# Kernel optimization log

Measured on AMD Instinct MI355X. Metric: run time of the kernel, lower is better.

Reference implementation:

```python
import jax, jax.numpy as jnp
import numpy as np

ROPE_THETA = 10000.0

def rope(x):
    # x: [B, H, T, D], D even. Standard rotate-half rotary embedding.
    T, D = x.shape[-2], x.shape[-1]
    half = D // 2
    inv_freq = 1.0 / (ROPE_THETA ** (jnp.arange(half, dtype=x.dtype) / half))
    ang = jnp.arange(T, dtype=x.dtype)[:, None] * inv_freq[None, :]  # [T, half]
    cos, sin = jnp.cos(ang), jnp.sin(ang)
    x1, x2 = x[..., :half], x[..., half:]
    return jnp.concatenate([x1 * cos - x2 * sin, x1 * sin + x2 * cos], axis=-1)


def setup_inputs() -> dict:
    key = jax.random.key(0)
    kq, kk, kv = jax.random.split(key, 3)
    shape = (2, 8, 4096, 64)  # [B, H, T, D]
    return {
        "Q": jax.random.normal(kq, shape, dtype=jnp.float32),
        "K": jax.random.normal(kk, shape, dtype=jnp.float32),
        "V": jax.random.normal(kv, shape, dtype=jnp.float32),
    }


def reference(Q, K, V):
    # Unnormalized causal linear attention with RoPE:
    #   tril(RoPE(Q) @ RoPE(K)^T, diagonal=-1) @ V
    Qr = rope(Q)
    Kr = rope(K)
    scores = jnp.einsum("bhqd,bhkd->bhqk", Qr, Kr)  # [B,H,T,T]
    T = scores.shape[-1]
    # strictly lower triangular (diagonal=-1): keep q_idx > k_idx
    mask = jnp.arange(T)[:, None] > jnp.arange(T)[None, :]
    scores = jnp.where(mask, scores, jnp.zeros((), dtype=scores.dtype))
    return jnp.einsum("bhqk,bhkd->bhqd", scores, V)
```

## Files before the change

### kernel.cpp

```cpp
#include <hip/hip_runtime.h>

#define G 16
#define T 4096
#define DD 64
#define NB 64

typedef __attribute__((ext_vector_type(8))) short bf16x8;
typedef __attribute__((ext_vector_type(4))) float f32x4;
typedef unsigned short U16;

__device__ __forceinline__ float bf2f(U16 u) {
  union { unsigned int u; float f; } x; x.u = ((unsigned int)u) << 16; return x.f;
}
__device__ __forceinline__ U16 f2bf(float f) {
  union { float f; unsigned int u; } x; x.f = f;
  unsigned int r = x.u + 0x7FFFu + ((x.u >> 16) & 1u);
  return (U16)(r >> 16);
}

#define MFMA(a, b, c) __builtin_amdgcn_mfma_f32_16x16x32_bf16((a), (b), (c), 0, 0, 0)

#define ROPE_C 0.28782313662425575f

__global__ __launch_bounds__(256) void k_tab(float2* __restrict__ tab) {
  int idx = blockIdx.x * 256 + threadIdx.x;
  int t = idx >> 5, j = idx & 31;
  float invf = expf(-(float)j * ROPE_C);
  float ang = (float)t * invf;
  tab[idx] = make_float2(cosf(ang), sinf(ang));
}

__global__ __launch_bounds__(256) void k_phase1(const float* __restrict__ K, const float* __restrict__ V,
                                                const float2* __restrict__ tab,
                                                U16* __restrict__ Kr, U16* __restrict__ Xu) {
  __shared__ __align__(16) U16 KrT[64][72];
  __shared__ __align__(16) U16 VT[64][72];
  int wid = blockIdx.x;
  int g = wid >> 6, b = wid & 63;
  int k0 = b * 64;
  int tid = threadIdx.x;

  {
    int r = tid >> 2, qq = tid & 3, d0 = qq * 8;
    int t = k0 + r;
    size_t base = ((size_t)g * T + t) * DD;
    const float* rp = K + base;
    const float2* tp = tab + t * 32 + d0;
    float x1[8], x2[8];
    *(float4*)&x1[0] = *(const float4*)(rp + d0);
    *(float4*)&x1[4] = *(const float4*)(rp + d0 + 4);
    *(float4*)&x2[0] = *(const float4*)(rp + d0 + 32);
    *(float4*)&x2[4] = *(const float4*)(rp + d0 + 36);
    bf16x8 v1, v2;
#pragma unroll
    for (int i = 0; i < 8; ++i) {
      float2 cs = tp[i];
      float o1 = x1[i] * cs.x - x2[i] * cs.y;
      float o2 = x1[i] * cs.y + x2[i] * cs.x;
      U16 b1 = f2bf(o1), b2 = f2bf(o2);
      v1[i] = (short)b1; v2[i] = (short)b2;
      KrT[d0 + i][r]      = b1;
      KrT[d0 + i + 32][r] = b2;
    }
    *(bf16x8*)(Kr + base + d0)      = v1;
    *(bf16x8*)(Kr + base + d0 + 32) = v2;
  }
  {
    int c = tid & 63, r0 = (tid >> 6) * 16;
#pragma unroll
    for (int h = 0; h < 2; ++h) {
      bf16x8 tv;
#pragma unroll
      for (int i = 0; i < 8; ++i)
        tv[i] = (short)f2bf(V[((size_t)g * T + k0 + r0 + h * 8 + i) * DD + c]);
      *(bf16x8*)&VT[c][r0 + h * 8] = tv;
    }
  }
  __syncthreads();

  int lane = tid & 63, wv = tid >> 6;
  int lr = lane & 15, lg = lane >> 4;
  bf16x8 A0 = *(const bf16x8*)&VT[16 * wv + lr][8 * lg];
  bf16x8 A1 = *(const bf16x8*)&VT[16 * wv + lr][8 * lg + 32];
#pragma unroll
  for (int dt = 0; dt < 4; ++dt) {
    bf16x8 B0 = *(const bf16x8*)&KrT[16 * dt + lr][8 * lg];
    bf16x8 B1 = *(const bf16x8*)&KrT[16 * dt + lr][8 * lg + 32];
    f32x4 acc = {0.f, 0.f, 0.f, 0.f};
    acc = MFMA(A0, B0, acc);
    acc = MFMA(A1, B1, acc);
#pragma unroll
    for (int rr = 0; rr < 4; ++rr) {
      int e = 16 * wv + 4 * lg + rr, d = 16 * dt + lr;
      Xu[((size_t)wid << 12) + e * 64 + d] = f2bf(acc[rr]);
    }
  }
}

__global__ __launch_bounds__(256) void k_phase2(U16* __restrict__ Xu) {
  int g = blockIdx.x >> 4, slice = blockIdx.x & 15;
  int e = slice * 256 + threadIdx.x;
  size_t base = ((size_t)g << 18) + e;
  float run = 0.f;
#pragma unroll
  for (int grp = 0; grp < 8; ++grp) {
    U16 v[8];
#pragma unroll
    for (int i = 0; i < 8; ++i)
      v[i] = Xu[base + ((size_t)(grp * 8 + i) << 12)];
#pragma unroll
    for (int i = 0; i < 8; ++i) {
      float f = bf2f(v[i]);
      Xu[base + ((size_t)(grp * 8 + i) << 12)] = f2bf(run);
      run += f;
    }
  }
}

__global__ __launch_bounds__(256) void k_phase3(const float* __restrict__ Q, const U16* __restrict__ Kr,
                                                const float* __restrict__ V, const U16* __restrict__ Xu,
                                                const float2* __restrict__ tab,
                                                float* __restrict__ Out) {
  __shared__ __align__(16) U16 SP[64][72];
  __shared__ __align__(16) U16 VT[64][72];
  __shared__ __align__(16) U16 SW[4][16][72];
  int wid = blockIdx.x;
  int g = wid >> 6, b = wid & 63;
  int k0 = b * 64;
  int tid = threadIdx.x;

  {
    int r = tid >> 2, c0 = (tid & 3) * 16;
    const U16* src = Xu + ((size_t)wid << 12) + r * 64 + c0;
    *(bf16x8*)&SP[r][c0]     = *(const bf16x8*)src;
    *(bf16x8*)&SP[r][c0 + 8] = *(const bf16x8*)(src + 8);
  }
  {
    int c = tid & 63, r0 = (tid >> 6) * 16;
#pragma unroll
    for (int h = 0; h < 2; ++h) {
      bf16x8 tv;
#pragma unroll
      for (int i = 0; i < 8; ++i)
        tv[i] = (short)f2bf(V[((size_t)g * T + k0 + r0 + h * 8 + i) * DD + c]);
      *(bf16x8*)&VT[c][r0 + h * 8] = tv;
    }
  }

  int lane = tid & 63, wv = tid >> 6;
  int lr = lane & 15, lg = lane >> 4;
  int q0 = k0 + 16 * wv;

  bf16x8 Aq0, Aq1;
  {
    int t = q0 + lr;
    const float* qrow = Q + ((size_t)g * T + t) * DD;
    const float2* tp = tab + t * 32 + 8 * lg;
    float x1[8], x2[8];
    *(float4*)&x1[0] = *(const float4*)(qrow + 8 * lg);
    *(float4*)&x1[4] = *(const float4*)(qrow + 8 * lg + 4);
    *(float4*)&x2[0] = *(const float4*)(qrow + 8 * lg + 32);
    *(float4*)&x2[4] = *(const float4*)(qrow + 8 * lg + 36);
#pragma unroll
    for (int i = 0; i < 8; ++i) {
      float2 cs = tp[i];
      Aq0[i] = (short)f2bf(x1[i] * cs.x - x2[i] * cs.y);
      Aq1[i] = (short)f2bf(x1[i] * cs.y + x2[i] * cs.x);
    }
  }
  __syncthreads();

  f32x4 O[4];
#pragma unroll
  for (int et = 0; et < 4; ++et) O[et] = (f32x4){0.f, 0.f, 0.f, 0.f};

#pragma unroll
  for (int et = 0; et < 4; ++et) {
    bf16x8 B0 = *(const bf16x8*)&SP[16 * et + lr][8 * lg];
    bf16x8 B1 = *(const bf16x8*)&SP[16 * et + lr][8 * lg + 32];
    O[et] = MFMA(Aq0, B0, O[et]);
    O[et] = MFMA(Aq1, B1, O[et]);
  }

  for (int kt = 0; kt <= wv; ++kt) {
    const U16* krow = Kr + ((size_t)g * T + k0 + 16 * kt + lr) * DD;
    bf16x8 Bk0 = *(const bf16x8*)(krow + 8 * lg);
    bf16x8 Bk1 = *(const bf16x8*)(krow + 8 * lg + 32);
    f32x4 s = {0.f, 0.f, 0.f, 0.f};
    s = MFMA(Aq0, Bk0, s);
    s = MFMA(Aq1, Bk1, s);
#pragma unroll
    for (int rr = 0; rr < 4; ++rr) {
      int qi = 16 * wv + 4 * lg + rr, ki = 16 * kt + lr;
      float val = (qi > ki) ? s[rr] : 0.f;
      SW[wv][4 * lg + rr][16 * kt + lr] = f2bf(val);
    }
  }
  for (int kt = wv + 1; kt < 4; ++kt) {
#pragma unroll
    for (int rr = 0; rr < 4; ++rr)
      SW[wv][4 * lg + rr][16 * kt + lr] = 0;
  }

  bf16x8 As0 = *(const bf16x8*)&SW[wv][lr][8 * lg];
  bf16x8 As1 = *(const bf16x8*)&SW[wv][lr][8 * lg + 32];

#pragma unroll
  for (int et = 0; et < 4; ++et) {
    bf16x8 Bv0 = *(const bf16x8*)&VT[16 * et + lr][8 * lg];
    bf16x8 Bv1 = *(const bf16x8*)&VT[16 * et + lr][8 * lg + 32];
    O[et] = MFMA(As0, Bv0, O[et]);
    O[et] = MFMA(As1, Bv1, O[et]);
  }

#pragma unroll
  for (int et = 0; et < 4; ++et)
#pragma unroll
    for (int rr = 0; rr < 4; ++rr)
      Out[((size_t)g * T + q0 + 4 * lg + rr) * DD + 16 * et + lr] = O[et][rr];
}

extern "C" void kernel_launch(void* const* d_in, const int* in_sizes, int n_in,
                              void* d_out, int out_size, void* d_ws, size_t ws_size,
                              hipStream_t stream) {
  const float* Q = (const float*)d_in[0];
  const float* K = (const float*)d_in[1];
  const float* V = (const float*)d_in[2];
  float* Out = (float*)d_out;
  U16* W  = (U16*)d_ws;
  U16* Kr = W;
  U16* Xu = W + 4194304;
  float2* tab = (float2*)(W + 8388608);
  k_tab<<<512, 256, 0, stream>>>(tab);
  k_phase1<<<G * NB, 256, 0, stream>>>(K, V, tab, Kr, Xu);
  k_phase2<<<256, 256, 0, stream>>>(Xu);
  k_phase3<<<G * NB, 256, 0, stream>>>(Q, Kr, V, Xu, tab, Out);
}
```

Measured before the change: 35.74 us.

## Compute RoPE inline, cache bf16 V, parallelize prefix scan across segments

Drops the separate cos/sin table kernel and computes the RoPE angles inline with fast __expf/__sincosf intrinsics, saving a launch and the table reads. Phase 1 now loads V with coalesced row vectors and writes a bf16 copy, which phase 3 reads instead of reconverting the fp32 V with strided loads. The prefix-sum kernel splits each 64-step chain into 4 segments of 16 combined by shuffles, giving four times more threads and a shorter serial chain. The fast trig intrinsics lose accuracy at large angles (t up to 4095), and the extra workspace buffer adds write traffic.

```diff
diff --git a/kernel.cpp b/kernel.cpp
--- a/kernel.cpp
+++ b/kernel.cpp
@@ -3,7 +3,6 @@
 #define G 16
 #define T 4096
 #define DD 64
-#define NB 64
 
 typedef __attribute__((ext_vector_type(8))) short bf16x8;
 typedef __attribute__((ext_vector_type(4))) float f32x4;
@@ -22,17 +21,9 @@
 
 #define ROPE_C 0.28782313662425575f
 
-__global__ __launch_bounds__(256) void k_tab(float2* __restrict__ tab) {
-  int idx = blockIdx.x * 256 + threadIdx.x;
-  int t = idx >> 5, j = idx & 31;
-  float invf = expf(-(float)j * ROPE_C);
-  float ang = (float)t * invf;
-  tab[idx] = make_float2(cosf(ang), sinf(ang));
-}
-
 __global__ __launch_bounds__(256) void k_phase1(const float* __restrict__ K, const float* __restrict__ V,
-                                                const float2* __restrict__ tab,
-                                                U16* __restrict__ Kr, U16* __restrict__ Xu) {
+                                                U16* __restrict__ Kr, U16* __restrict__ Vb,
+                                                U16* __restrict__ Xu) {
   __shared__ __align__(16) U16 KrT[64][72];
   __shared__ __align__(16) U16 VT[64][72];
   int wid = blockIdx.x;
@@ -40,12 +31,12 @@
   int k0 = b * 64;
   int tid = threadIdx.x;
 
-  {
-    int r = tid >> 2, qq = tid & 3, d0 = qq * 8;
-    int t = k0 + r;
-    size_t base = ((size_t)g * T + t) * DD;
+  int r = tid >> 2, qq = tid & 3, d0 = qq * 8;
+  int t = k0 + r;
+  size_t base = ((size_t)g * T + t) * DD;
+
+  {
     const float* rp = K + base;
-    const float2* tp = tab + t * 32 + d0;
     float x1[8], x2[8];
     *(float4*)&x1[0] = *(const float4*)(rp + d0);
     *(float4*)&x1[4] = *(const float4*)(rp + d0 + 4);
@@ -54,9 +45,12 @@
     bf16x8 v1, v2;
 #pragma unroll
     for (int i = 0; i < 8; ++i) {
-      float2 cs = tp[i];
-      float o1 = x1[i] * cs.x - x2[i] * cs.y;
-      float o2 = x1[i] * cs.y + x2[i] * cs.x;
+      float invf = __expf(-(float)(d0 + i) * ROPE_C);
+      float ang = (float)t * invf;
+      float s, c;
+      __sincosf(ang, &s, &c);
+      float o1 = x1[i] * c - x2[i] * s;
+      float o2 = x1[i] * s + x2[i] * c;
       U16 b1 = f2bf(o1), b2 = f2bf(o2);
       v1[i] = (short)b1; v2[i] = (short)b2;
       KrT[d0 + i][r]      = b1;
@@ -66,15 +60,22 @@
     *(bf16x8*)(Kr + base + d0 + 32) = v2;
   }
   {
-    int c = tid & 63, r0 = (tid >> 6) * 16;
-#pragma unroll
-    for (int h = 0; h < 2; ++h) {
-      bf16x8 tv;
-#pragma unroll
-      for (int i = 0; i < 8; ++i)
-        tv[i] = (short)f2bf(V[((size_t)g * T + k0 + r0 + h * 8 + i) * DD + c]);
-      *(bf16x8*)&VT[c][r0 + h * 8] = tv;
-    }
+    const float* vp = V + base;
+    float y1[8], y2[8];
+    *(float4*)&y1[0] = *(const float4*)(vp + d0);
+    *(float4*)&y1[4] = *(const float4*)(vp + d0 + 4);
+    *(float4*)&y2[0] = *(const float4*)(vp + d0 + 32);
+    *(float4*)&y2[4] = *(const float4*)(vp + d0 + 36);
+    bf16x8 w1, w2;
+#pragma unroll
+    for (int i = 0; i < 8; ++i) {
+      U16 b1 = f2bf(y1[i]), b2 = f2bf(y2[i]);
+      w1[i] = (short)b1; w2[i] = (short)b2;
+      VT[d0 + i][r]      = b1;
+      VT[d0 + i + 32][r] = b2;
+    }
+    *(bf16x8*)(Vb + base + d0)      = w1;
+    *(bf16x8*)(Vb + base + d0 + 32) = w2;
   }
   __syncthreads();
 
@@ -97,29 +98,35 @@
   }
 }
 
-__global__ __launch_bounds__(256) void k_phase2(U16* __restrict__ Xu) {
-  int g = blockIdx.x >> 4, slice = blockIdx.x & 15;
-  int e = slice * 256 + threadIdx.x;
-  size_t base = ((size_t)g << 18) + e;
+__global__ __launch_bounds__(256) void k_phase2b(U16* __restrict__ Xu) {
+  int tau = blockIdx.x * 256 + threadIdx.x;
+  int chain = tau >> 2, seg = tau & 3;
+  int hd = chain >> 12, col = chain & 4095;
+  size_t base = ((size_t)hd << 18) + ((size_t)(seg * 16) << 12) + col;
+  U16 v[16];
+#pragma unroll
+  for (int i = 0; i < 16; ++i)
+    v[i] = Xu[base + ((size_t)i << 12)];
+  float s = 0.f;
+#pragma unroll
+  for (int i = 0; i < 16; ++i) s += bf2f(v[i]);
+  float b1 = __shfl_up(s, 1, 4);
+  float b2 = __shfl_up(s, 2, 4);
+  float b3 = __shfl_up(s, 3, 4);
   float run = 0.f;
-#pragma unroll
-  for (int grp = 0; grp < 8; ++grp) {
-    U16 v[8];
-#pragma unroll
-    for (int i = 0; i < 8; ++i)
-      v[i] = Xu[base + ((size_t)(grp * 8 + i) << 12)];
-#pragma unroll
-    for (int i = 0; i < 8; ++i) {
-      float f = bf2f(v[i]);
-      Xu[base + ((size_t)(grp * 8 + i) << 12)] = f2bf(run);
-      run += f;
-    }
+  if (seg > 0) run += b1;
+  if (seg > 1) run += b2;
+  if (seg > 2) run += b3;
+#pragma unroll
+  for (int i = 0; i < 16; ++i) {
+    float f = bf2f(v[i]);
+    Xu[base + ((size_t)i << 12)] = f2bf(run);
+    run += f;
   }
 }
 
 __global__ __launch_bounds__(256) void k_phase3(const float* __restrict__ Q, const U16* __restrict__ Kr,
-                                                const float* __restrict__ V, const U16* __restrict__ Xu,
-                                                const float2* __restrict__ tab,
+                                                const U16* __restrict__ Vb, const U16* __restrict__ Xu,
                                                 float* __restrict__ Out) {
   __shared__ __align__(16) U16 SP[64][72];
   __shared__ __align__(16) U16 VT[64][72];
@@ -136,14 +143,14 @@
     *(bf16x8*)&SP[r][c0 + 8] = *(const bf16x8*)(src + 8);
   }
   {
-    int c = tid & 63, r0 = (tid >> 6) * 16;
-#pragma unroll
-    for (int h = 0; h < 2; ++h) {
-      bf16x8 tv;
-#pragma unroll
-      for (int i = 0; i < 8; ++i)
-        tv[i] = (short)f2bf(V[((size_t)g * T + k0 + r0 + h * 8 + i) * DD + c]);
-      *(bf16x8*)&VT[c][r0 + h * 8] = tv;
+    int r = tid >> 2, qq = tid & 3, d0 = qq * 8;
+    size_t base = ((size_t)g * T + k0 + r) * DD;
+    bf16x8 a0 = *(const bf16x8*)(Vb + base + d0);
+    bf16x8 a1 = *(const bf16x8*)(Vb + base + d0 + 32);
+#pragma unroll
+    for (int i = 0; i < 8; ++i) {
+      VT[d0 + i][r]      = (U16)a0[i];
+      VT[d0 + i + 32][r] = (U16)a1[i];
     }
   }
 
@@ -155,7 +162,6 @@
   {
     int t = q0 + lr;
     const float* qrow = Q + ((size_t)g * T + t) * DD;
-    const float2* tp = tab + t * 32 + 8 * lg;
     float x1[8], x2[8];
     *(float4*)&x1[0] = *(const float4*)(qrow + 8 * lg);
     *(float4*)&x1[4] = *(const float4*)(qrow + 8 * lg + 4);
@@ -163,9 +169,12 @@
     *(float4*)&x2[4] = *(const float4*)(qrow + 8 * lg + 36);
 #pragma unroll
     for (int i = 0; i < 8; ++i) {
-      float2 cs = tp[i];
-      Aq0[i] = (short)f2bf(x1[i] * cs.x - x2[i] * cs.y);
-      Aq1[i] = (short)f2bf(x1[i] * cs.y + x2[i] * cs.x);
+      float invf = __expf(-(float)(8 * lg + i) * ROPE_C);
+      float ang = (float)t * invf;
+      float s, c;
+      __sincosf(ang, &s, &c);
+      Aq0[i] = (short)f2bf(x1[i] * c - x2[i] * s);
+      Aq1[i] = (short)f2bf(x1[i] * s + x2[i] * c);
     }
   }
   __syncthreads();
@@ -229,10 +238,9 @@
   float* Out = (float*)d_out;
   U16* W  = (U16*)d_ws;
   U16* Kr = W;
-  U16* Xu = W + 4194304;
-  float2* tab = (float2*)(W + 8388608);
-  k_tab<<<512, 256, 0, stream>>>(tab);
-  k_phase1<<<G * NB, 256, 0, stream>>>(K, V, tab, Kr, Xu);
-  k_phase2<<<256, 256, 0, stream>>>(Xu);
-  k_phase3<<<G * NB, 256, 0, stream>>>(Q, Kr, V, Xu, tab, Out);
-}
+  U16* Vb = W + 4194304;
+  U16* Xu = W + 8388608;
+  k_phase1<<<G * 64, 256, 0, stream>>>(K, V, Kr, Vb, Xu);
+  k_phase2b<<<1024, 256, 0, stream>>>(Xu);
+  k_phase3<<<G * 64, 256, 0, stream>>>(Q, Kr, Vb, Xu, Out);
+}
```

Result: faster. 32.14 us (-10.1%).
